# Kernel optimization log

Measured on AMD Instinct MI355X. Metric: run time of the kernel, lower is better.

The kernel has to match this reference:

```python
import jax, jax.numpy as jnp
import numpy as np

B, S, D, H = 2, 2048, 1024, 16
HD = D // H  # head_dim = 64


def setup_inputs() -> dict:
    key = jax.random.key(0)
    ks = jax.random.split(key, 9)
    xav = float(np.sqrt(6.0 / (D + D)))  # xavier_uniform bound for square matrices
    def lin_w(k):
        return jax.random.uniform(k, (D, D), jnp.float32, -xav, xav)
    return {
        "x": jax.random.normal(ks[0], (B, S, D), jnp.float32),
        "mask": jnp.ones((B, S), jnp.int32),
        "Wq": lin_w(ks[1]), "bq": jnp.zeros((D,), jnp.float32),
        "Wk": lin_w(ks[2]), "bk": jnp.zeros((D,), jnp.float32),
        "Wv": lin_w(ks[3]), "bv": jnp.zeros((D,), jnp.float32),
        "Wo": lin_w(ks[4]), "bo": jnp.zeros((D,), jnp.float32),
    }


def reference(x, mask, Wq, bq, Wk, bk, Wv, bv, Wo, bo):
    # Linear projections (torch Linear: y = x @ W.T + b)
    q = x @ Wq.T + bq
    k = x @ Wk.T + bk
    v = x @ Wv.T + bv
    # [B, S, D] -> [B, H, S, HD]
    q = q.reshape(B, S, H, HD).transpose(0, 2, 1, 3)
    k = k.reshape(B, S, H, HD).transpose(0, 2, 1, 3)
    v = v.reshape(B, S, H, HD).transpose(0, 2, 1, 3)
    scores = jnp.einsum("bhqd,bhkd->bhqk", q, k) / jnp.sqrt(jnp.float32(HD))
    # mask [B, S] -> [B, 1, 1, S]; masked_fill where mask == 0
    m = mask[:, None, None, :]
    scores = jnp.where(m == 0, jnp.float32(-1e9), scores)
    attn = jax.nn.softmax(scores, axis=-1)
    # dropout in eval mode = identity
    out = jnp.einsum("bhqk,bhkd->bhqd", attn, v)
    out = out.transpose(0, 2, 1, 3).reshape(B, S, D)
    return out @ Wo.T + bo
```

## Files before the change

### kernel.cpp

```cpp
#include <hip/hip_runtime.h>
#include <stdint.h>

#define B_   2
#define S_   2048
#define D_   1024
#define H_   16
#define HD_  64
#define NTOK (B_ * S_)

typedef unsigned short u16;
typedef __bf16 bf16x8 __attribute__((ext_vector_type(8)));
typedef float  f32x4  __attribute__((ext_vector_type(4)));
typedef u16    u16x4  __attribute__((ext_vector_type(4)));

#define QSCALE 0.180336880f
#define MAXC 4.0f

#if __has_builtin(__builtin_amdgcn_exp2f)
#define EXP2(x) __builtin_amdgcn_exp2f(x)
#else
#define EXP2(x) exp2f(x)
#endif

#define OFF_FLAG ((size_t)0)
#define OFF_BIAS ((size_t)64)
#define OFF_MB   ((size_t)32768)
#define OFF_MF   ((size_t)49152)
#define OFF_X    ((size_t)65536)
#define SZ_X     ((size_t)NTOK * D_ * 2)
#define OFF_W    (OFF_X + SZ_X)
#define SZ_W     ((size_t)D_ * D_ * 2)
#define OFF_Q    (OFF_W + 4 * SZ_W)
#define SZ_T     SZ_X
#define OFF_K2   (OFF_Q + SZ_T)
#define OFF_VT   (OFF_K2 + SZ_T)
#define OFF_AO   (OFF_VT + SZ_T)

__device__ __forceinline__ float bf2f(u16 h) {
    union { uint32_t u; float f; } c; c.u = ((uint32_t)h) << 16; return c.f;
}
__device__ __forceinline__ u16 f2bf(float f) {
    union { float f; uint32_t u; } c; c.f = f;
    uint32_t r = c.u + 0x7fffu + ((c.u >> 16) & 1u);
    return (u16)(r >> 16);
}
__device__ __forceinline__ void glds16(const u16* g, u16* l) {
    __builtin_amdgcn_global_load_lds(
        (const __attribute__((address_space(1))) uint32_t*)g,
        (__attribute__((address_space(3))) uint32_t*)l,
        16, 0, 0);
}
__device__ __forceinline__ f32x4 mfma16(bf16x8 a, bf16x8 b, f32x4 c) {
    return __builtin_amdgcn_mfma_f32_16x16x32_bf16(a, b, c, 0, 0, 0);
}
__device__ __forceinline__ uint32_t pk_bf_trunc(float f0, float f1) {
    return __builtin_amdgcn_perm(__builtin_bit_cast(uint32_t, f1),
                                 __builtin_bit_cast(uint32_t, f0), 0x07060302u);
}

__global__ void convert_kernel(const void* x, const void* wq, const void* wk,
                               const void* wv, const void* wo,
                               const void* bq, const void* bk, const void* bv,
                               const void* bo, const int* mask, char* ws) {
    __shared__ int s_ok;
    const int tid = threadIdx.x;
    if (tid == 0) s_ok = 1;
    __syncthreads();
    {
        const u16* p = (const u16*)wq;
        bool bad = false;
        for (int j = 0; j < 8; ++j) {
            float v = bf2f(p[(tid * 8 + j) * 2]);
            if (!(v > -1.0f && v < 1.0f)) bad = true;
        }
        if (bad) s_ok = 0;
    }
    __syncthreads();
    const int is_bf16 = s_ok;
    if (blockIdx.x == 0 && tid == 0) *(int*)(ws + OFF_FLAG) = is_bf16;

    const uint32_t NX = (uint32_t)NTOK * D_;
    const uint32_t NW = (uint32_t)D_ * D_;
    if (!is_bf16) {
        u16* Xd = (u16*)(ws + OFF_X);
        u16* Wd = (u16*)(ws + OFF_W);
        for (uint32_t i = blockIdx.x * 256u + tid; i < NX + 4 * NW;
             i += gridDim.x * 256u) {
            const void* src; uint32_t si; u16* dst;
            if (i < NX) { src = x; si = i; dst = Xd + i; }
            else {
                uint32_t j = i - NX;
                uint32_t w = j >> 20; si = j & (NW - 1u);
                src = (w == 0) ? wq : (w == 1) ? wk : (w == 2) ? wv : wo;
                dst = Wd + j;
            }
            *dst = f2bf(((const float*)src)[si]);
        }
    }
    float* Bd = (float*)(ws + OFF_BIAS);
    float* Mbd = (float*)(ws + OFF_MB);
    int* MFd = (int*)(ws + OFF_MF);
    const uint32_t NB = 4u * D_;
    const uint32_t total2 = NB + (uint32_t)NTOK + B_ * 32;
    for (uint32_t i = blockIdx.x * 256u + tid; i < total2;
         i += gridDim.x * 256u) {
        if (i < NB) {
            uint32_t w = i >> 10; uint32_t si = i & (D_ - 1u);
            const void* src = (w == 0) ? bq : (w == 1) ? bk : (w == 2) ? bv : bo;
            Bd[i] = is_bf16 ? bf2f(((const u16*)src)[si]) : ((const float*)src)[si];
        } else if (i < NB + (uint32_t)NTOK) {
            uint32_t j = i - NB;
            Mbd[j] = (mask[j] == 0) ? -1.0e9f : 0.0f;
        } else {
            uint32_t f = i - NB - (uint32_t)NTOK;
            uint32_t bb = f >> 5, kt = f & 31;
            int any = 0;
            for (int e = 0; e < 64; ++e)
                any |= (mask[bb * S_ + kt * 64 + e] == 0);
            MFd[f] = any;
        }
    }
}

__global__ void qkv_gemm(char* ws, const void* x, const void* wq,
                         const void* wk, const void* wv) {
    __shared__ alignas(16) u16 As[128 * 32];
    __shared__ alignas(16) u16 Bs[128 * 32];
    const int z = blockIdx.z;
    const int is_bf16 = *(const int*)(ws + OFF_FLAG);
    const u16* X = is_bf16 ? (const u16*)x : (const u16*)(ws + OFF_X);
    const u16* W;
    if (is_bf16) W = (z == 0) ? (const u16*)wq : (z == 1) ? (const u16*)wk : (const u16*)wv;
    else         W = (const u16*)(ws + OFF_W + (size_t)z * SZ_W);
    const float* bias = (const float*)(ws + OFF_BIAS) + z * D_;
    u16* Qd  = (u16*)(ws + OFF_Q);
    u16* Kd  = (u16*)(ws + OFF_K2);
    u16* Vtd = (u16*)(ws + OFF_VT);

    const int tid = threadIdx.x, lane = tid & 63, wave = tid >> 6;
    const int wm = (wave & 1) * 64, wn = (wave >> 1) * 64;
    const int lr = lane & 15, quad = lane >> 4;
    const int srow = tid >> 2;
    const int scol = (((tid & 3) ^ ((tid >> 3) & 3)) * 8);
    const int rd_off = (quad ^ ((lr >> 1) & 3)) * 8;

    const u16* Araw; const u16* Braw; int m0, n0;
    if (z < 2) { Araw = W; Braw = X; m0 = blockIdx.x * 128; n0 = blockIdx.y * 128; }
    else       { Araw = X; Braw = W; m0 = blockIdx.y * 128; n0 = blockIdx.x * 128; }

    f32x4 acc[4][4];
#pragma unroll
    for (int i = 0; i < 4; i++)
#pragma unroll
        for (int j = 0; j < 4; j++) acc[i][j] = (f32x4){0.f, 0.f, 0.f, 0.f};

    const u16* Ag0 = Araw + (size_t)(m0 + srow)      * D_ + scol;
    const u16* Ag1 = Araw + (size_t)(m0 + srow + 64) * D_ + scol;
    const u16* Bg0 = Braw + (size_t)(n0 + srow)      * D_ + scol;
    const u16* Bg1 = Braw + (size_t)(n0 + srow + 64) * D_ + scol;

    for (int k0 = 0; k0 < D_; k0 += 32) {
        glds16(Ag0 + k0, &As[tid * 8]);
        glds16(Ag1 + k0, &As[2048 + tid * 8]);
        glds16(Bg0 + k0, &Bs[tid * 8]);
        glds16(Bg1 + k0, &Bs[2048 + tid * 8]);
        __syncthreads();
        bf16x8 a[4], b[4];
#pragma unroll
        for (int i = 0; i < 4; i++) a[i] = *(const bf16x8*)&As[(wm + i * 16 + lr) * 32 + rd_off];
#pragma unroll
        for (int j = 0; j < 4; j++) b[j] = *(const bf16x8*)&Bs[(wn + j * 16 + lr) * 32 + rd_off];
#pragma unroll
        for (int i = 0; i < 4; i++)
#pragma unroll
            for (int j = 0; j < 4; j++) acc[i][j] = mfma16(a[i], b[j], acc[i][j]);
        __syncthreads();
    }

    if (z < 2) {
        u16* dst0 = (z == 0) ? Qd : Kd;
        const float sc_ = (z == 0) ? QSCALE : 1.0f;
#pragma unroll
        for (int i = 0; i < 4; i++) {
            const int fb = m0 + wm + i * 16 + quad * 4;
            const f32x4 b4 = *(const f32x4*)&bias[fb];
            const int h = fb >> 6, hd0 = fb & 63;
#pragma unroll
            for (int j = 0; j < 4; j++) {
                const int tok = n0 + wn + j * 16 + lr;
                const int bb = tok >> 11, s = tok & 2047;
                u16x4 pk;
#pragma unroll
                for (int r = 0; r < 4; r++) pk[r] = f2bf((acc[i][j][r] + b4[r]) * sc_);
                *(u16x4*)&dst0[(((size_t)(bb * H_ + h)) * S_ + s) * HD_ + hd0] = pk;
            }
        }
    } else {
#pragma unroll
        for (int i = 0; i < 4; i++) {
            const int row_b = m0 + wm + i * 16 + quad * 4;
            const int bb = row_b >> 11, s0 = row_b & 2047;
#pragma unroll
            for (int j = 0; j < 4; j++) {
                const int col = n0 + wn + j * 16 + lr;
                const float bv_ = bias[col];
                const int h = col >> 6, hd = col & 63;
                u16x4 pk;
#pragma unroll
                for (int r = 0; r < 4; r++) pk[r] = f2bf(acc[i][j][r] + bv_);
                *(u16x4*)&Vtd[(((size_t)(bb * H_ + h)) * HD_ + hd) * S_ + s0] = pk;
            }
        }
    }
}

__global__ void __launch_bounds__(256)
attn_kernel(char* ws) {
    __shared__ alignas(16) char smem[49152];

    const u16* Qb  = (const u16*)(ws + OFF_Q);
    const u16* Kb  = (const u16*)(ws + OFF_K2);
    const u16* Vtb = (const u16*)(ws + OFF_VT);
    const float* Mb = (const float*)(ws + OFF_MB);
    const int* MF = (const int*)(ws + OFF_MF);
    u16* AO = (u16*)(ws + OFF_AO);

    const int tid = threadIdx.x, lane = tid & 63, wave = tid >> 6;
    const int kc = wave >> 1, qhalf = wave & 1;
    const int bh = blockIdx.y, b = bh >> 4, h = bh & 15;
    const int qb = blockIdx.x * 64 + qhalf * 32;
    const int lr = lane & 15, quad = lane >> 4;
    const int sx = lr & 7;

    const u16* Qbh = Qb  + (size_t)bh * S_ * HD_;
    const u16* Kbh = Kb  + (size_t)bh * S_ * HD_;
    const u16* Vbh = Vtb + (size_t)bh * HD_ * S_;
    const float* Mbb = Mb + b * S_;
    const int* MFb = MF + b * 32;

    u16* Ks  = (u16*)(smem + kc * 8192);
    u16* Vts = (u16*)(smem + 16384 + kc * 8192);
    u16* Pw  = (u16*)(smem + 32768 + wave * 4096);

    const int tidh = tid & 127;
    const int st_r = tidh >> 3;
    const int st_c = (tidh & 7) ^ (st_r & 7);
    const u16* Kst = Kbh + (size_t)(kc * 1024 + st_r) * HD_ + st_c * 8;
    const u16* Vst = Vbh + (size_t)st_r * S_ + kc * 1024 + st_c * 8;

    bf16x8 qf[2][2];
#pragma unroll
    for (int s = 0; s < 2; ++s)
#pragma unroll
        for (int hf = 0; hf < 2; ++hf)
            qf[s][hf] = *(const bf16x8*)&Qbh[(size_t)(qb + s * 16 + lr) * HD_ + hf * 32 + quad * 8];

    bf16x8 ones8;
#pragma unroll
    for (int i = 0; i < 8; ++i) ones8[i] = (__bf16)1.0f;

    f32x4 oacc[2][4], lacc[2];
#pragma unroll
    for (int s = 0; s < 2; ++s) {
        lacc[s] = (f32x4){0.f, 0.f, 0.f, 0.f};
#pragma unroll
        for (int j = 0; j < 4; ++j) oacc[s][j] = (f32x4){0.f, 0.f, 0.f, 0.f};
    }

    for (int it = 0; it < 16; ++it) {
        const int k0 = kc * 1024 + it * 64;
#pragma unroll
        for (int t = 0; t < 4; ++t) {
            glds16(Kst + (size_t)(it * 64 + t * 16) * HD_, &Ks[(tidh + t * 128) * 8]);
            glds16(Vst + (size_t)t * 16 * S_ + it * 64,    &Vts[(tidh + t * 128) * 8]);
        }
        __syncthreads();

        f32x4 sc[2][4];
#pragma unroll
        for (int j = 0; j < 4; ++j) {
            const int krow = (j * 16 + lr) * 64;
            bf16x8 kfA = *(const bf16x8*)&Ks[krow + ((quad    ) ^ sx) * 8];
            bf16x8 kfB = *(const bf16x8*)&Ks[krow + ((quad + 4) ^ sx) * 8];
#pragma unroll
            for (int s = 0; s < 2; ++s) {
                f32x4 t0 = mfma16(kfA, qf[s][0], (f32x4){0.f, 0.f, 0.f, 0.f});
                sc[s][j] = mfma16(kfB, qf[s][1], t0);
            }
        }
        if (MFb[kc * 16 + it]) {
#pragma unroll
            for (int j = 0; j < 4; ++j) {
                const f32x4 mb = *(const f32x4*)&Mbb[k0 + j * 16 + quad * 4];
#pragma unroll
                for (int s = 0; s < 2; ++s) sc[s][j] += mb;
            }
        }
        bf16x8 vf[4][2];
#pragma unroll
        for (int j2 = 0; j2 < 4; ++j2) {
            const int vrow = (j2 * 16 + lr) * 64;
            vf[j2][0] = *(const bf16x8*)&Vts[vrow + ((quad    ) ^ sx) * 8];
            vf[j2][1] = *(const bf16x8*)&Vts[vrow + ((quad + 4) ^ sx) * 8];
        }

#pragma unroll
        for (int s = 0; s < 2; ++s) {
            const int prow = (s * 16 + lr) * 64;
#pragma unroll
            for (int j = 0; j < 4; ++j) {
                f32x4 p;
#pragma unroll
                for (int r = 0; r < 4; ++r) p[r] = EXP2(sc[s][j][r] - MAXC);
                uint2 pk;
                pk.x = pk_bf_trunc(p[0], p[1]);
                pk.y = pk_bf_trunc(p[2], p[3]);
                *(uint2*)&Pw[prow + (((2 * j + (quad >> 1)) ^ sx) * 8) + (quad & 1) * 4] = pk;
            }
            bf16x8 pf0 = *(const bf16x8*)&Pw[prow + ((quad    ) ^ sx) * 8];
            bf16x8 pf1 = *(const bf16x8*)&Pw[prow + ((quad + 4) ^ sx) * 8];
            lacc[s] = mfma16(ones8, pf0, lacc[s]);
            lacc[s] = mfma16(ones8, pf1, lacc[s]);
#pragma unroll
            for (int j2 = 0; j2 < 4; ++j2) {
                oacc[s][j2] = mfma16(vf[j2][0], pf0, oacc[s][j2]);
                oacc[s][j2] = mfma16(vf[j2][1], pf1, oacc[s][j2]);
            }
        }
        __syncthreads();
    }

    float* Oex = (float*)smem;
    float* lex = (float*)(smem + 17408);
    if (kc == 1) {
#pragma unroll
        for (int s = 0; s < 2; ++s) {
            const int row = qhalf * 32 + s * 16 + lr;
#pragma unroll
            for (int j2 = 0; j2 < 4; ++j2)
                *(f32x4*)&Oex[row * 68 + j2 * 16 + quad * 4] = oacc[s][j2];
            if (quad == 0) lex[row] = lacc[s][0];
        }
    }
    __syncthreads();
    if (kc == 0) {
#pragma unroll
        for (int s = 0; s < 2; ++s) {
            const int row = qhalf * 32 + s * 16 + lr;
            const float linv = 1.0f / (lacc[s][0] + lex[row]);
            const int q = qb + s * 16 + lr;
            u16* dst = AO + (size_t)(b * S_ + q) * D_ + h * HD_ + quad * 4;
#pragma unroll
            for (int j2 = 0; j2 < 4; ++j2) {
                const f32x4 o2 = *(const f32x4*)&Oex[row * 68 + j2 * 16 + quad * 4];
                u16x4 pk;
#pragma unroll
                for (int r = 0; r < 4; ++r) pk[r] = f2bf((oacc[s][j2][r] + o2[r]) * linv);
                *(u16x4*)&dst[j2 * 16] = pk;
            }
        }
    }
}

__global__ void out_gemm(char* ws, const void* wo, void* dout) {
    __shared__ alignas(16) u16 As[128 * 32];
    __shared__ alignas(16) u16 Bs[64 * 32];
    const int is_bf16 = *(const int*)(ws + OFF_FLAG);
    const u16* A  = (const u16*)(ws + OFF_AO);
    const u16* Bt = is_bf16 ? (const u16*)wo : (const u16*)(ws + OFF_W + 3 * SZ_W);
    const float* bias = (const float*)(ws + OFF_BIAS) + 3 * D_;

    const int tid = threadIdx.x, lane = tid & 63, wave = tid >> 6;
    const int wm = (wave & 1) * 64, wn = (wave >> 1) * 32;
    const int m0 = blockIdx.y * 128, n0 = blockIdx.x * 64;
    const int lr = lane & 15, quad = lane >> 4;
    const int srow = tid >> 2;
    const int scol = (((tid & 3) ^ ((tid >> 3) & 3)) * 8);
    const int rd_off = (quad ^ ((lr >> 1) & 3)) * 8;

    f32x4 acc[4][2];
#pragma unroll
    for (int i = 0; i < 4; i++)
#pragma unroll
        for (int j = 0; j < 2; j++) acc[i][j] = (f32x4){0.f, 0.f, 0.f, 0.f};

    const u16* Ag0 = A  + (size_t)(m0 + srow)      * D_ + scol;
    const u16* Ag1 = A  + (size_t)(m0 + srow + 64) * D_ + scol;
    const u16* Bg0 = Bt + (size_t)(n0 + srow)      * D_ + scol;

    for (int k0 = 0; k0 < D_; k0 += 32) {
        glds16(Ag0 + k0, &As[tid * 8]);
        glds16(Ag1 + k0, &As[2048 + tid * 8]);
        glds16(Bg0 + k0, &Bs[tid * 8]);
        __syncthreads();
        bf16x8 a[4], b[2];
#pragma unroll
        for (int i = 0; i < 4; i++) a[i] = *(const bf16x8*)&As[(wm + i * 16 + lr) * 32 + rd_off];
#pragma unroll
        for (int j = 0; j < 2; j++) b[j] = *(const bf16x8*)&Bs[(wn + j * 16 + lr) * 32 + rd_off];
#pragma unroll
        for (int i = 0; i < 4; i++)
#pragma unroll
            for (int j = 0; j < 2; j++) acc[i][j] = mfma16(a[i], b[j], acc[i][j]);
        __syncthreads();
    }
#pragma unroll
    for (int i = 0; i < 4; i++) {
        const int row_b = m0 + wm + i * 16 + quad * 4;
#pragma unroll
        for (int j = 0; j < 2; j++) {
            const int col = n0 + wn + j * 16 + lr;
            const float bv_ = bias[col];
#pragma unroll
            for (int r = 0; r < 4; r++) {
                const int row = row_b + r;
                const float v = acc[i][j][r] + bv_;
                const size_t idx = (size_t)row * D_ + col;
                if (is_bf16) ((u16*)dout)[idx] = f2bf(v);
                else         ((float*)dout)[idx] = v;
            }
        }
    }
}

extern "C" void kernel_launch(void* const* d_in, const int* in_sizes, int n_in,
                              void* d_out, int out_size, void* d_ws, size_t ws_size,
                              hipStream_t stream) {
    (void)in_sizes; (void)n_in; (void)out_size; (void)ws_size;
    const void* x  = d_in[0];
    const int* mask = (const int*)d_in[1];
    const void* wq = d_in[2]; const void* bq = d_in[3];
    const void* wk = d_in[4]; const void* bk = d_in[5];
    const void* wv = d_in[6]; const void* bv = d_in[7];
    const void* wo = d_in[8]; const void* bo = d_in[9];
    char* ws = (char*)d_ws;

    convert_kernel<<<dim3(2048), dim3(256), 0, stream>>>(x, wq, wk, wv, wo,
                                                         bq, bk, bv, bo, mask, ws);
    qkv_gemm<<<dim3(8, 32, 3), dim3(256), 0, stream>>>(ws, x, wq, wk, wv);
    attn_kernel<<<dim3(S_ / 64, B_ * H_), dim3(256), 0, stream>>>(ws);
    out_gemm<<<dim3(16, 32), dim3(256), 0, stream>>>(ws, wo, d_out);
}
```

Before: 230.1 us.

## Restructure attention loop to cut registers and LDS, raise occupancy, shrink convert grid

The attention kernel now computes scores, mask add, exp and P-write per (s, j) tile instead of holding all scores first. This lets the per-wave P staging buffer shrink to one 16-row slice, cutting LDS from 48KB to 40KB, and a launch bound of 4 blocks per CU is added. The convert kernel grid goes from 2048 to 128 blocks, and EXP2 now always uses exp2f instead of the amdgcn builtin. Higher occupancy is meant to hide latency, at the risk of register spills, and the smaller convert grid may change that kernel's throughput.

```diff
diff --git a/kernel.cpp b/kernel.cpp
--- a/kernel.cpp
+++ b/kernel.cpp
@@ -16,11 +16,7 @@
 #define QSCALE 0.180336880f
 #define MAXC 4.0f
 
-#if __has_builtin(__builtin_amdgcn_exp2f)
-#define EXP2(x) __builtin_amdgcn_exp2f(x)
-#else
 #define EXP2(x) exp2f(x)
-#endif
 
 #define OFF_FLAG ((size_t)0)
 #define OFF_BIAS ((size_t)64)
@@ -214,9 +210,9 @@
     }
 }
 
-__global__ void __launch_bounds__(256)
+__global__ void __launch_bounds__(256, 4)
 attn_kernel(char* ws) {
-    __shared__ alignas(16) char smem[49152];
+    __shared__ alignas(16) char smem[40960];
 
     const u16* Qb  = (const u16*)(ws + OFF_Q);
     const u16* Kb  = (const u16*)(ws + OFF_K2);
@@ -240,7 +236,7 @@
 
     u16* Ks  = (u16*)(smem + kc * 8192);
     u16* Vts = (u16*)(smem + 16384 + kc * 8192);
-    u16* Pw  = (u16*)(smem + 32768 + wave * 4096);
+    u16* Pw  = (u16*)(smem + 32768 + wave * 2048);
 
     const int tidh = tid & 127;
     const int st_r = tidh >> 3;
@@ -276,42 +272,34 @@
         }
         __syncthreads();
 
-        f32x4 sc[2][4];
+        bf16x8 kf[4][2], vf[4][2];
 #pragma unroll
         for (int j = 0; j < 4; ++j) {
             const int krow = (j * 16 + lr) * 64;
-            bf16x8 kfA = *(const bf16x8*)&Ks[krow + ((quad    ) ^ sx) * 8];
-            bf16x8 kfB = *(const bf16x8*)&Ks[krow + ((quad + 4) ^ sx) * 8];
-#pragma unroll
-            for (int s = 0; s < 2; ++s) {
-                f32x4 t0 = mfma16(kfA, qf[s][0], (f32x4){0.f, 0.f, 0.f, 0.f});
-                sc[s][j] = mfma16(kfB, qf[s][1], t0);
-            }
-        }
-        if (MFb[kc * 16 + it]) {
+            kf[j][0] = *(const bf16x8*)&Ks[krow + ((quad    ) ^ sx) * 8];
+            kf[j][1] = *(const bf16x8*)&Ks[krow + ((quad + 4) ^ sx) * 8];
+            vf[j][0] = *(const bf16x8*)&Vts[krow + ((quad    ) ^ sx) * 8];
+            vf[j][1] = *(const bf16x8*)&Vts[krow + ((quad + 4) ^ sx) * 8];
+        }
+        const int masked = MFb[kc * 16 + it];
+        f32x4 mb[4];
+        if (masked) {
+#pragma unroll
+            for (int j = 0; j < 4; ++j)
+                mb[j] = *(const f32x4*)&Mbb[k0 + j * 16 + quad * 4];
+        }
+
+#pragma unroll
+        for (int s = 0; s < 2; ++s) {
+            const int prow = lr * 64;
 #pragma unroll
             for (int j = 0; j < 4; ++j) {
-                const f32x4 mb = *(const f32x4*)&Mbb[k0 + j * 16 + quad * 4];
-#pragma unroll
-                for (int s = 0; s < 2; ++s) sc[s][j] += mb;
-            }
-        }
-        bf16x8 vf[4][2];
-#pragma unroll
-        for (int j2 = 0; j2 < 4; ++j2) {
-            const int vrow = (j2 * 16 + lr) * 64;
-            vf[j2][0] = *(const bf16x8*)&Vts[vrow + ((quad    ) ^ sx) * 8];
-            vf[j2][1] = *(const bf16x8*)&Vts[vrow + ((quad + 4) ^ sx) * 8];
-        }
-
-#pragma unroll
-        for (int s = 0; s < 2; ++s) {
-            const int prow = (s * 16 + lr) * 64;
-#pragma unroll
-            for (int j = 0; j < 4; ++j) {
+                f32x4 t0 = mfma16(kf[j][0], qf[s][0], (f32x4){0.f, 0.f, 0.f, 0.f});
+                f32x4 scj = mfma16(kf[j][1], qf[s][1], t0);
+                if (masked) scj += mb[j];
                 f32x4 p;
 #pragma unroll
-                for (int r = 0; r < 4; ++r) p[r] = EXP2(sc[s][j][r] - MAXC);
+                for (int r = 0; r < 4; ++r) p[r] = EXP2(scj[r] - MAXC);
                 uint2 pk;
                 pk.x = pk_bf_trunc(p[0], p[1]);
                 pk.y = pk_bf_trunc(p[2], p[3]);
@@ -435,8 +423,8 @@
     const void* wo = d_in[8]; const void* bo = d_in[9];
     char* ws = (char*)d_ws;
 
-    convert_kernel<<<dim3(2048), dim3(256), 0, stream>>>(x, wq, wk, wv, wo,
-                                                         bq, bk, bv, bo, mask, ws);
+    convert_kernel<<<dim3(128), dim3(256), 0, stream>>>(x, wq, wk, wv, wo,
+                                                        bq, bk, bv, bo, mask, ws);
     qkv_gemm<<<dim3(8, 32, 3), dim3(256), 0, stream>>>(ws, x, wq, wk, wv);
     attn_kernel<<<dim3(S_ / 64, B_ * H_), dim3(256), 0, stream>>>(ws);
     out_gemm<<<dim3(16, 32), dim3(256), 0, stream>>>(ws, wo, d_out);
```

New measurement: 505.7 us. +119.8%, slower.
